# Kernel tuning notes

Hardware: AMD Instinct MI355X
Metric: run time of the kernel (lower is better)

## Reference

```python
import jax, jax.numpy as jnp
import numpy as np
from jax import lax

E = 5          # experts
CIN = 256      # in_planes
COUT = 256     # out_planes
K = 3          # kernel_size
HID = CIN // 4 + 1  # attention hidden dim
STRIDE = 1
PAD = 1


def setup_inputs() -> dict:
    key = jax.random.key(0)
    k_x, k_w, k_a1, k_a2 = jax.random.split(key, 4)
    B, H, W = 32, 56, 56
    x = jax.random.normal(k_x, (B, CIN, H, W), dtype=jnp.float32)
    # expert conv weights (E, O, I, K, K), kaiming-uniform-ish scale
    fan_in = CIN * K * K
    bound = float(np.sqrt(6.0 / fan_in))
    weight = jax.random.uniform(k_w, (E, COUT, CIN, K, K), dtype=jnp.float32,
                                minval=-bound, maxval=bound)
    # align_conv initialized as per-expert identity mixing matrix (E, O, O)
    align_mat = jnp.tile(jnp.eye(COUT, dtype=jnp.float32)[None], (E, 1, 1))
    # attention MLP (1x1 convs on pooled features == matmuls)
    att_w1 = jax.random.normal(k_a1, (HID, CIN), dtype=jnp.float32) * float(np.sqrt(2.0 / CIN))
    att_w2 = jax.random.normal(k_a2, (E, HID), dtype=jnp.float32) * float(np.sqrt(2.0 / HID))
    att_b2 = jnp.zeros((E,), dtype=jnp.float32)
    return {"x": x, "weight": weight, "align_mat": align_mat,
            "att_w1": att_w1, "att_w2": att_w2, "att_b2": att_b2}


def _ada_agg_forward(x, weight, align_mat, att_w1, att_w2, att_b2):
    # attention: global avg pool -> 1x1 conv -> relu -> 1x1 conv -> sigmoid
    s = jnp.mean(x, axis=(2, 3))                      # (B, CIN)
    h = jax.nn.relu(jnp.einsum('bc,hc->bh', s, att_w1))  # (B, HID)
    attn = jax.nn.sigmoid(jnp.einsum('bh,eh->be', h, att_w2) + att_b2)  # (B, E)

    # align: per-expert channel remix of expert weights
    # W'_e[j] = sum_o align_mat[e, j, o] * W_e[o]
    w_aligned = jnp.einsum('ejo,eoixy->ejixy', align_mat, weight)  # (E, O, I, K, K)

    # per-sample aggregated weights
    agg_w = jnp.einsum('be,eoixy->boixy', attn, w_aligned)  # (B, O, I, K, K)

    # per-sample conv (the torch groups=batch trick), vectorized with vmap
    def conv_one(xi, wi):
        # xi: (CIN, H, W), wi: (O, I, K, K)
        return lax.conv_general_dilated(
            xi[None], wi,
            window_strides=(STRIDE, STRIDE),
            padding=((PAD, PAD), (PAD, PAD)),
            dimension_numbers=('NCHW', 'OIHW', 'NCHW'))[0]

    return jax.vmap(conv_one)(x, agg_w)  # (B, O, H', W')


def reference(x, weight, align_mat, att_w1, att_w2, att_b2):
    return _ada_agg_forward(x, weight, align_mat, att_w1, att_w2, att_b2)
```

## Files before the change

kernel.cpp:

```cpp
#include <hip/hip_runtime.h>
#include <hip/hip_bf16.h>

#define BATCH 32
#define CIN   256
#define COUT  256
#define HH    56
#define HP    58
#define NEXP  5
#define HID   65

#define OFF_S     0
#define OFF_ATTN  32768
#define OFF_WAL   65536
#define OFF_AGGW  (12u*1024u*1024u)
#define OFF_XPAD  (48u*1024u*1024u)

typedef __bf16 bf16x8 __attribute__((ext_vector_type(8)));
typedef float  f32x4  __attribute__((ext_vector_type(4)));

__device__ __forceinline__ unsigned short f2bf(float f) {
    unsigned int u = __float_as_uint(f);
    unsigned int r = (u + 0x7FFFu + ((u >> 16) & 1u)) >> 16;
    return (unsigned short)r;
}

#define AS1 __attribute__((address_space(1)))
#define AS3 __attribute__((address_space(3)))
__device__ __forceinline__ void gl_lds16(const unsigned short* g, unsigned short* l) {
    __builtin_amdgcn_global_load_lds((const AS1 void*)g, (AS3 void*)l, 16, 0, 0);
}

#define XLP 132
__global__ void xprep_kernel(const float* __restrict__ x,
                             unsigned short* __restrict__ xpad,
                             float* __restrict__ s) {
    const int y0 = blockIdx.x * 2, c0 = blockIdx.y * 128, b = blockIdx.z;
    const int tid = threadIdx.x, lane = tid & 63, wg = tid >> 6;
    __shared__ unsigned short lds[2 * HH * XLP];

    {
        const uint4 z = make_uint4(0, 0, 0, 0);
        if (blockIdx.x == 0) {
            uint4* p = (uint4*)(xpad + (size_t)(b * HP * HP) * 256 + c0);
            for (int i = tid; i < HP * 16; i += 256)
                p[(i >> 4) * 32 + (i & 15)] = z;
        }
        if (blockIdx.x == 27) {
            uint4* p = (uint4*)(xpad + (size_t)((b * HP + 57) * HP) * 256 + c0);
            for (int i = tid; i < HP * 16; i += 256)
                p[(i >> 4) * 32 + (i & 15)] = z;
        }
        if (tid < 64) {
            const int r = y0 + 1 + (tid >> 5);
            const int cc = ((tid >> 4) & 1) * 57;
            uint4* p = (uint4*)(xpad + (size_t)((b * HP + r) * HP + cc) * 256 + c0);
            p[tid & 15] = z;
        }
    }

    #pragma unroll 2
    for (int cc = wg; cc < 128; cc += 4) {
        if (lane < HH) {
            const float2 v = *(const float2*)&x[
                (size_t)((b * 256 + c0 + cc) * HH + y0) * HH + lane * 2];
            const int p = lane * 2;
            const int r0 = p / HH, x0 = p - r0 * HH;
            const int q = p + 1;
            const int r1 = q / HH, x1 = q - r1 * HH;
            lds[(r0 * HH + x0) * XLP + cc] = f2bf(v.x);
            lds[(r1 * HH + x1) * XLP + cc] = f2bf(v.y);
        }
    }
    __syncthreads();
    {
        const int r = tid >> 7, c = tid & 127;
        float sum = 0.f;
        for (int xx = 0; xx < HH; ++xx) {
            const unsigned int u = lds[(r * HH + xx) * XLP + c];
            sum += __uint_as_float(u << 16);
        }
        atomicAdd(&s[b * 256 + c0 + c], sum);
    }
    for (int i = tid; i < 2 * HH * 32; i += 256) {
        const int r = (i >= HH * 32) ? 1 : 0;
        const int rem = i - r * HH * 32;
        const int xx = rem >> 5, cq = (rem & 31) * 4;
        const uint2 v = *(const uint2*)&lds[(r * HH + xx) * XLP + cq];
        *(uint2*)(xpad + (size_t)(((b * HP + y0 + r + 1) * HP + (xx + 1))) * 256
                  + c0 + cq) = v;
    }
}

__global__ void attn_kernel(const float* __restrict__ s,
                            const float* __restrict__ w1,
                            const float* __restrict__ w2,
                            const float* __restrict__ b2,
                            float* __restrict__ attn) {
    const int b = blockIdx.x, tid = threadIdx.x;
    __shared__ float sm[256];
    __shared__ float part[130];
    __shared__ float hm[HID];
    sm[tid] = s[b * 256 + tid] * (1.f / 3136.f);
    __syncthreads();
    if (tid < 130) {
        const int h = (tid >= 65) ? tid - 65 : tid;
        const int base = (tid >= 65) ? 128 : 0;
        float acc = 0.f;
        #pragma unroll 4
        for (int c = 0; c < 128; ++c) acc += sm[base + c] * w1[h * 256 + base + c];
        part[tid] = acc;
    }
    __syncthreads();
    if (tid < HID) hm[tid] = fmaxf(part[tid] + part[tid + 65], 0.f);
    __syncthreads();
    if (tid < NEXP) {
        float acc = b2[tid];
        for (int j = 0; j < HID; ++j) acc += hm[j] * w2[tid * HID + j];
        attn[b * NEXP + tid] = 1.f / (1.f + expf(-acc));
    }
}

__global__ void align_kernel(const float* __restrict__ am,
                             const float* __restrict__ w,
                             float* __restrict__ wal) {
    const int nt = blockIdx.x, jt = blockIdx.y, e = blockIdx.z;
    const int tid = threadIdx.x;
    const int tj = tid >> 5, tn = tid & 31;
    __shared__ float At[64][33];
    __shared__ float Wt[32][128];
    float acc[8][4];
    #pragma unroll
    for (int a = 0; a < 8; ++a)
        #pragma unroll
        for (int c = 0; c < 4; ++c) acc[a][c] = 0.f;

    for (int o0 = 0; o0 < 256; o0 += 32) {
        {
            const int row = tid >> 2, col = (tid & 3) * 8;
            const float* src = am + (size_t)((e * 256) + jt * 64 + row) * 256 + o0 + col;
            float4 v0 = *(const float4*)(src);
            float4 v1 = *(const float4*)(src + 4);
            *(float4*)&At[row][col] = v0;
            *(float4*)&At[row][col + 4] = v1;
        }
        {
            const int row = tid >> 3, col = (tid & 7) * 16;
            const float* src = w + (size_t)((e * 256) + o0 + row) * 2304 + nt * 128 + col;
            #pragma unroll
            for (int q = 0; q < 4; ++q)
                *(float4*)&Wt[row][col + q * 4] = *(const float4*)(src + q * 4);
        }
        __syncthreads();
        for (int k = 0; k < 32; ++k) {
            float wv[4];
            #pragma unroll
            for (int c = 0; c < 4; ++c) wv[c] = Wt[k][tn * 4 + c];
            #pragma unroll
            for (int a = 0; a < 8; ++a) {
                const float av = At[tj * 8 + a][k];
                #pragma unroll
                for (int c = 0; c < 4; ++c) acc[a][c] += av * wv[c];
            }
        }
        __syncthreads();
    }
    #pragma unroll
    for (int a = 0; a < 8; ++a) {
        const int j = jt * 64 + tj * 8 + a;
        #pragma unroll
        for (int c = 0; c < 4; ++c) {
            const int n = nt * 128 + tn * 4 + c;
            const int t = n % 9, i = n / 9;
            wal[(size_t)(((e * 9 + t) * 256 + j)) * 256 + i] = acc[a][c];
        }
    }
}

__global__ void agg_kernel(const float* __restrict__ wal,
                           const float* __restrict__ attn,
                           unsigned short* __restrict__ aggw) {
    const int t = blockIdx.x >> 6;
    const int j = (blockIdx.x & 63) * 4 + (threadIdx.x >> 6);
    const int i = (threadIdx.x & 63) * 4;
    __shared__ float at[BATCH * NEXP];
    if (threadIdx.x < BATCH * NEXP) at[threadIdx.x] = attn[threadIdx.x];
    float4 wv[NEXP];
    #pragma unroll
    for (int e = 0; e < NEXP; ++e)
        wv[e] = *(const float4*)&wal[(size_t)(((e * 9 + t) * 256 + j)) * 256 + i];
    __syncthreads();
    for (int b = 0; b < BATCH; ++b) {
        float4 acc = make_float4(0.f, 0.f, 0.f, 0.f);
        #pragma unroll
        for (int e = 0; e < NEXP; ++e) {
            const float a = at[b * NEXP + e];
            acc.x += a * wv[e].x; acc.y += a * wv[e].y;
            acc.z += a * wv[e].z; acc.w += a * wv[e].w;
        }
        uint2 pk;
        pk.x = (unsigned)f2bf(acc.x) | ((unsigned)f2bf(acc.y) << 16);
        pk.y = (unsigned)f2bf(acc.z) | ((unsigned)f2bf(acc.w) << 16);
        *(uint2*)&aggw[(size_t)(((b * 9 + t) * 256 + j)) * 256 + i] = pk;
    }
}

__global__ __launch_bounds__(256, 2) void conv_kernel(
        const unsigned short* __restrict__ xpad,
        const unsigned short* __restrict__ aggw,
        float* __restrict__ out) {
    const int blk = blockIdx.x;
    const int xcd = blk & 7, slot = blk >> 3;
    const int b = xcd * 4 + slot / 28;
    const int pos = slot % 28;
    const int y0 = (pos / 7) * 14, x0 = (pos % 7) * 8;
    const int tid = threadIdx.x;
    const int wave = tid >> 6, lane = tid & 63;
    const int quad = lane >> 4, ln = lane & 15;

    __shared__ unsigned short lds[2 * 640 * 8];

    f32x4 acc[4][7];
    #pragma unroll
    for (int mt = 0; mt < 4; ++mt)
        #pragma unroll
        for (int nt = 0; nt < 7; ++nt) acc[mt][nt] = (f32x4){0.f, 0.f, 0.f, 0.f};

    int nb[7];
    #pragma unroll
    for (int nt = 0; nt < 7; ++nt)
        nb[nt] = ((((ln >> 3) + nt * 2) * 40 + (ln & 7) * 4 + quad)) * 16;

    const unsigned short* ap0 = aggw +
        (size_t)(b * 9 * 65536 + (wave * 64 + ln) * 256 + quad * 8);

    const unsigned short* sp[3];
    int ldsu[3];
    #pragma unroll
    for (int k = 0; k < 3; ++k) {
        int u = tid + k * 256; if (u > 639) u = 639;
        const int r = u / 40, rem = u - r * 40;
        const int c = rem >> 2, sub = rem & 3;
        sp[k] = xpad + (size_t)(((b * HP + y0 + r) * HP + x0 + c)) * 256 + sub * 8;
        ldsu[k] = u * 8;
    }

    gl_lds16(sp[0], lds + ldsu[0]);
    gl_lds16(sp[1], lds + ldsu[1]);
    if (tid < 128) gl_lds16(sp[2], lds + ldsu[2]);
    __syncthreads();

    int pp = 0;
    #pragma unroll 2
    for (int c0 = 0; c0 < 256; c0 += 32) {
        if (c0 < 224) {
            unsigned short* dst = lds + (pp ^ 1) * 5120;
            gl_lds16(sp[0] + c0 + 32, dst + ldsu[0]);
            gl_lds16(sp[1] + c0 + 32, dst + ldsu[1]);
            if (tid < 128) gl_lds16(sp[2] + c0 + 32, dst + ldsu[2]);
        }
        const char* lb = (const char*)lds + pp * 10240;
        #pragma unroll
        for (int ky = 0; ky < 3; ++ky) {
            #pragma unroll
            for (int kx = 0; kx < 3; ++kx) {
                const int tap = ky * 3 + kx;
                const unsigned short* ap = ap0 + tap * 65536 + c0;
                bf16x8 a[4];
                #pragma unroll
                for (int mt = 0; mt < 4; ++mt)
                    a[mt] = *(const bf16x8*)(ap + mt * 16 * 256);
                #pragma unroll
                for (int nt = 0; nt < 7; ++nt) {
                    const bf16x8 bf = *(const bf16x8*)(lb +
                        nb[nt] + (ky * 40 + kx * 4) * 16);
                    #pragma unroll
                    for (int mt = 0; mt < 4; ++mt)
                        acc[mt][nt] = __builtin_amdgcn_mfma_f32_16x16x32_bf16(
                            a[mt], bf, acc[mt][nt], 0, 0, 0);
                }
            }
        }
        __syncthreads();
        pp ^= 1;
    }

    #pragma unroll
    for (int mt = 0; mt < 4; ++mt) {
        #pragma unroll
        for (int nt = 0; nt < 7; ++nt) {
            const int yy = y0 + (ln >> 3) + nt * 2;
            const int xx = x0 + (ln & 7);
            #pragma unroll
            for (int r = 0; r < 4; ++r) {
                const int cout = wave * 64 + mt * 16 + quad * 4 + r;
                out[(size_t)(((b * 256 + cout) * HH + yy)) * HH + xx] = acc[mt][nt][r];
            }
        }
    }
}

extern "C" void kernel_launch(void* const* d_in, const int* in_sizes, int n_in,
                              void* d_out, int out_size, void* d_ws, size_t ws_size,
                              hipStream_t stream) {
    const float* x      = (const float*)d_in[0];
    const float* weight = (const float*)d_in[1];
    const float* am     = (const float*)d_in[2];
    const float* w1     = (const float*)d_in[3];
    const float* w2     = (const float*)d_in[4];
    const float* b2     = (const float*)d_in[5];
    float* out = (float*)d_out;
    char* ws = (char*)d_ws;

    float* s             = (float*)(ws + OFF_S);
    float* attn          = (float*)(ws + OFF_ATTN);
    float* wal           = (float*)(ws + OFF_WAL);
    unsigned short* aggw = (unsigned short*)(ws + OFF_AGGW);
    unsigned short* xpad = (unsigned short*)(ws + OFF_XPAD);

    hipMemsetAsync(s, 0, BATCH * 256 * sizeof(float), stream);
    xprep_kernel<<<dim3(28, 2, BATCH), 256, 0, stream>>>(x, xpad, s);
    attn_kernel<<<BATCH, 256, 0, stream>>>(s, w1, w2, b2, attn);
    align_kernel<<<dim3(18, 4, NEXP), 256, 0, stream>>>(am, weight, wal);
    agg_kernel<<<576, 256, 0, stream>>>(wal, attn, aggw);
    conv_kernel<<<896, 256, 0, stream>>>(xpad, aggw, out);
}
```

Before: 423.9 us.

## Stage per-sample weights in LDS and double spatial tile per block

Conv blocks grow to 512 threads (8 waves) and cover a 28x8 spatial tile. The aggregated weight slices, three taps at a time, are staged into LDS with async global-to-LDS copies and double buffered. Before, each wave loaded its A fragments straight from global memory, so weights were fetched redundantly by every block of the same sample; sharing them in LDS across two spatial wave groups halves that traffic. The cost is about 137KB of dynamic LDS, which limits occupancy, plus a barrier for every tap group, giving three syncs per channel chunk instead of one.

```diff
diff --git a/kernel.cpp b/kernel.cpp
--- a/kernel.cpp
+++ b/kernel.cpp
@@ -204,20 +204,27 @@
     }
 }
 
-__global__ __launch_bounds__(256, 2) void conv_kernel(
+#define CONV_LDSB_U16 19200
+#define CONV_LDSA_U16 49152
+#define CONV_LDS_BYTES ((CONV_LDSB_U16 + CONV_LDSA_U16) * 2)
+__global__ __launch_bounds__(512, 2) void conv_kernel(
         const unsigned short* __restrict__ xpad,
         const unsigned short* __restrict__ aggw,
         float* __restrict__ out) {
     const int blk = blockIdx.x;
     const int xcd = blk & 7, slot = blk >> 3;
-    const int b = xcd * 4 + slot / 28;
-    const int pos = slot % 28;
-    const int y0 = (pos / 7) * 14, x0 = (pos % 7) * 8;
+    const int b = xcd * 4 + slot / 14;
+    const int pos = slot % 14;
+    const int x0 = (pos >> 1) * 8;
+    const int y0 = (pos & 1) * 28;
     const int tid = threadIdx.x;
-    const int wave = tid >> 6, lane = tid & 63;
+    const int w = tid >> 6, lane = tid & 63;
+    const int wm = w & 3, wp = w >> 2;
     const int quad = lane >> 4, ln = lane & 15;
 
-    __shared__ unsigned short lds[2 * 640 * 8];
+    extern __shared__ unsigned short smem[];
+    unsigned short* ldsB = smem;
+    unsigned short* ldsA = smem + CONV_LDSB_U16;
 
     f32x4 acc[4][7];
     #pragma unroll
@@ -228,71 +235,93 @@
     int nb[7];
     #pragma unroll
     for (int nt = 0; nt < 7; ++nt)
-        nb[nt] = ((((ln >> 3) + nt * 2) * 40 + (ln & 7) * 4 + quad)) * 16;
-
-    const unsigned short* ap0 = aggw +
-        (size_t)(b * 9 * 65536 + (wave * 64 + ln) * 256 + quad * 8);
-
-    const unsigned short* sp[3];
-    int ldsu[3];
+        nb[nt] = (((wp * 14 + (ln >> 3) + nt * 2) * 40 + (ln & 7) * 4 + quad)) * 16;
+
+    const int abase = ((wm * 64 + ln) * 4 + quad) * 16;
+
+    const unsigned short* bsp[3];
+    int bldsu[3];
     #pragma unroll
     for (int k = 0; k < 3; ++k) {
-        int u = tid + k * 256; if (u > 639) u = 639;
+        int u = tid + k * 512; if (u > 1199) u = 1199;
         const int r = u / 40, rem = u - r * 40;
         const int c = rem >> 2, sub = rem & 3;
-        sp[k] = xpad + (size_t)(((b * HP + y0 + r) * HP + x0 + c)) * 256 + sub * 8;
-        ldsu[k] = u * 8;
-    }
-
-    gl_lds16(sp[0], lds + ldsu[0]);
-    gl_lds16(sp[1], lds + ldsu[1]);
-    if (tid < 128) gl_lds16(sp[2], lds + ldsu[2]);
-    __syncthreads();
-
-    int pp = 0;
-    #pragma unroll 2
+        bsp[k] = xpad + (size_t)(((b * HP + y0 + r) * HP + x0 + c)) * 256 + sub * 8;
+        bldsu[k] = u * 8;
+    }
+    const unsigned short* asp[6];
+    int aldsu[6];
+    #pragma unroll
+    for (int k = 0; k < 6; ++k) {
+        const int u = tid + k * 512;
+        const int tl = u >> 10, rem = u & 1023;
+        const int cout = rem >> 2, sub = rem & 3;
+        asp[k] = aggw + ((size_t)(b * 9 + tl) * 256 + cout) * 256 + sub * 8;
+        aldsu[k] = u * 8;
+    }
+
+    {
+        gl_lds16(bsp[0], ldsB + bldsu[0]);
+        gl_lds16(bsp[1], ldsB + bldsu[1]);
+        if (tid < 176) gl_lds16(bsp[2], ldsB + bldsu[2]);
+        #pragma unroll
+        for (int k = 0; k < 6; ++k) gl_lds16(asp[k], ldsA + aldsu[k]);
+    }
+    __syncthreads();
+
+    int pa = 0, pb = 0;
+    #pragma unroll 1
     for (int c0 = 0; c0 < 256; c0 += 32) {
-        if (c0 < 224) {
-            unsigned short* dst = lds + (pp ^ 1) * 5120;
-            gl_lds16(sp[0] + c0 + 32, dst + ldsu[0]);
-            gl_lds16(sp[1] + c0 + 32, dst + ldsu[1]);
-            if (tid < 128) gl_lds16(sp[2] + c0 + 32, dst + ldsu[2]);
-        }
-        const char* lb = (const char*)lds + pp * 10240;
-        #pragma unroll
-        for (int ky = 0; ky < 3; ++ky) {
-            #pragma unroll
-            for (int kx = 0; kx < 3; ++kx) {
-                const int tap = ky * 3 + kx;
-                const unsigned short* ap = ap0 + tap * 65536 + c0;
+        #pragma unroll
+        for (int tg = 0; tg < 3; ++tg) {
+            if (tg < 2) {
+                unsigned short* dA = ldsA + (pa ^ 1) * 24576;
+                const int off = (tg + 1) * 196608 + c0;
+                #pragma unroll
+                for (int k = 0; k < 6; ++k) gl_lds16(asp[k] + off, dA + aldsu[k]);
+            } else if (c0 < 224) {
+                unsigned short* dA = ldsA + (pa ^ 1) * 24576;
+                const int off = c0 + 32;
+                #pragma unroll
+                for (int k = 0; k < 6; ++k) gl_lds16(asp[k] + off, dA + aldsu[k]);
+                unsigned short* dB = ldsB + (pb ^ 1) * 9600;
+                gl_lds16(bsp[0] + c0 + 32, dB + bldsu[0]);
+                gl_lds16(bsp[1] + c0 + 32, dB + bldsu[1]);
+                if (tid < 176) gl_lds16(bsp[2] + c0 + 32, dB + bldsu[2]);
+            }
+            const char* lB = (const char*)ldsB + pb * 19200;
+            const char* lA = (const char*)ldsA + pa * 49152;
+            #pragma unroll
+            for (int tl = 0; tl < 3; ++tl) {
                 bf16x8 a[4];
                 #pragma unroll
                 for (int mt = 0; mt < 4; ++mt)
-                    a[mt] = *(const bf16x8*)(ap + mt * 16 * 256);
+                    a[mt] = *(const bf16x8*)(lA + tl * 16384 + mt * 1024 + abase);
                 #pragma unroll
                 for (int nt = 0; nt < 7; ++nt) {
-                    const bf16x8 bf = *(const bf16x8*)(lb +
-                        nb[nt] + (ky * 40 + kx * 4) * 16);
+                    const bf16x8 bf = *(const bf16x8*)(lB +
+                        nb[nt] + (tg * 40 + tl * 4) * 16);
                     #pragma unroll
                     for (int mt = 0; mt < 4; ++mt)
                         acc[mt][nt] = __builtin_amdgcn_mfma_f32_16x16x32_bf16(
                             a[mt], bf, acc[mt][nt], 0, 0, 0);
                 }
             }
-        }
-        __syncthreads();
-        pp ^= 1;
+            __syncthreads();
+            pa ^= 1;
+        }
+        pb ^= 1;
     }
 
     #pragma unroll
     for (int mt = 0; mt < 4; ++mt) {
         #pragma unroll
         for (int nt = 0; nt < 7; ++nt) {
-            const int yy = y0 + (ln >> 3) + nt * 2;
+            const int yy = y0 + wp * 14 + (ln >> 3) + nt * 2;
             const int xx = x0 + (ln & 7);
             #pragma unroll
             for (int r = 0; r < 4; ++r) {
-                const int cout = wave * 64 + mt * 16 + quad * 4 + r;
+                const int cout = wm * 64 + mt * 16 + quad * 4 + r;
                 out[(size_t)(((b * 256 + cout) * HH + yy)) * HH + xx] = acc[mt][nt][r];
             }
         }
@@ -317,10 +346,18 @@
     unsigned short* aggw = (unsigned short*)(ws + OFF_AGGW);
     unsigned short* xpad = (unsigned short*)(ws + OFF_XPAD);
 
+    static bool attr_set = false;
+    if (!attr_set) {
+        hipFuncSetAttribute((const void*)conv_kernel,
+                            hipFuncAttributeMaxDynamicSharedMemorySize,
+                            CONV_LDS_BYTES);
+        attr_set = true;
+    }
+
     hipMemsetAsync(s, 0, BATCH * 256 * sizeof(float), stream);
     xprep_kernel<<<dim3(28, 2, BATCH), 256, 0, stream>>>(x, xpad, s);
     attn_kernel<<<BATCH, 256, 0, stream>>>(s, w1, w2, b2, attn);
     align_kernel<<<dim3(18, 4, NEXP), 256, 0, stream>>>(am, weight, wal);
     agg_kernel<<<576, 256, 0, stream>>>(wal, attn, aggw);
-    conv_kernel<<<896, 256, 0, stream>>>(xpad, aggw, out);
-}
+    conv_kernel<<<448, 512, CONV_LDS_BYTES, stream>>>(xpad, aggw, out);
+}
```

After: 378.0 us. 10.8% less time.
